# Performance work log

Hardware: AMD Instinct MI355X
Metric: run time of the kernel (lower is better)

## Reference

```python
import jax, jax.numpy as jnp
import numpy as np

N = 16384          # number of units
K = 655
BOOST_STRENGTH = 1.0


def setup_inputs() -> dict:
    key = jax.random.key(0)
    k1, k2 = jax.random.split(key)
    x = jax.random.normal(k1, (4096, N), dtype=jnp.float32)
    dutyCycle = jax.random.uniform(k2, (N,), dtype=jnp.float32)
    return {"x": x, "dutyCycle": dutyCycle}


def reference(x, dutyCycle):
    # boost factor per unit: encourages under-used units
    targetDensity = K / x.shape[1]
    boostFactors = jnp.exp((targetDensity - dutyCycle) * BOOST_STRENGTH)  # (N,)
    boosted = x * boostFactors  # (B, N)
    # top-k per row, then scatter a binary mask of winners
    _, idx = jax.lax.top_k(boosted, K)  # (B, K)
    b = jnp.arange(x.shape[0])[:, None]  # (B, 1)
    res = jnp.zeros_like(x).at[b, idx].set(1.0)
    return res
```

## Files before the change

kernel.cpp:

```cpp
#include <hip/hip_runtime.h>
#include <math.h>
#include <stdint.h>


#define N_UNITS 16384
#define K_WIN 655
#define NT 512
#define NPROBE 11
#define CAP 2048
#define ITERS (N_UNITS / (NT * 4))

__device__ __forceinline__ uint32_t fkey(float f) {
    uint32_t b = __float_as_uint(f);
    uint32_t m = (uint32_t)((int32_t)b >> 31) | 0x80000000u;
    return b ^ m;
}

__global__ void boost_kernel(const float* __restrict__ duty,
                             float* __restrict__ bf, int n) {
    int i = blockIdx.x * blockDim.x + threadIdx.x;
    if (i < n) {
        const float td = 0.03997802734375f;
        float s = td - duty[i];
        bf[i] = (float)exp((double)s);
    }
}

__global__ __launch_bounds__(NT, 6) void kwinners_kernel(
    const float* __restrict__ x, const float* __restrict__ bf,
    float* __restrict__ out) {
    __shared__ uint32_t red[(NT / 64) * NPROBE];
    __shared__ int cglob[NPROBE];
    __shared__ int prb[NPROBE];
    __shared__ uint32_t cand_idx[CAP];
    __shared__ uint32_t cand_key[CAP];
    __shared__ int sc[1];

    const int tid = threadIdx.x;
    const int lane = tid & 63;
    const int w = tid >> 6;
    const int row = blockIdx.x;
    const float4* xrow = (const float4*)(x + (size_t)row * N_UNITS);
    const float4* bfv = (const float4*)bf;
    float* orow = out + (size_t)row * N_UNITS;

    if (tid == 0) sc[0] = 0;

    int P[NPROBE];
    {
        const float pv[NPROBE] = {1.90f, 1.70f, 1.55f, 1.43f, 1.33f, 1.25f,
                                  1.18f, 1.12f, 1.06f, 0.99f, 0.90f};
#pragma unroll
        for (int p = 0; p < NPROBE; ++p) P[p] = (int)(fkey(pv[p]) >> 16);
    }

    int cnt[NPROBE];
#pragma unroll
    for (int p = 0; p < NPROBE; ++p) cnt[p] = 0;

    uint2 kh[ITERS];

#pragma unroll
    for (int j = 0; j < ITERS; ++j) {
        int i4 = tid + j * NT;
        float4 xv = xrow[i4];
        float4 bv = bfv[i4];
        int h0 = (int)(fkey(xv.x * bv.x) >> 16);
        int h1 = (int)(fkey(xv.y * bv.y) >> 16);
        int h2 = (int)(fkey(xv.z * bv.z) >> 16);
        int h3 = (int)(fkey(xv.w * bv.w) >> 16);
        kh[j].x = (uint32_t)h0 | ((uint32_t)h1 << 16);
        kh[j].y = (uint32_t)h2 | ((uint32_t)h3 << 16);
#pragma unroll
        for (int p = 0; p < NPROBE; ++p)
            cnt[p] += __popcll(__ballot(h0 > P[p])) +
                      __popcll(__ballot(h1 > P[p])) +
                      __popcll(__ballot(h2 > P[p])) +
                      __popcll(__ballot(h3 > P[p]));
    }

    auto reduce_counts = [&]() {
        if (lane == 0) {
#pragma unroll
            for (int p = 0; p < NPROBE; ++p)
                red[w * NPROBE + p] = (uint32_t)cnt[p];
        }
        __syncthreads();
        if (tid < NPROBE) {
            int s = 0;
#pragma unroll
            for (int ww = 0; ww < NT / 64; ++ww) s += (int)red[ww * NPROBE + tid];
            cglob[tid] = s;
        }
        __syncthreads();
    };
    reduce_counts();

    int lo, hi, cab, cgl;
    {
        int j = 0;
        while (j < NPROBE && cglob[j] < K_WIN) ++j;
        if (j == 0) {
            lo = P[0]; cgl = cglob[0]; hi = 65535; cab = 0;
        } else if (j == NPROBE) {
            lo = -1; cgl = N_UNITS; hi = P[NPROBE - 1]; cab = cglob[NPROBE - 1];
        } else {
            lo = P[j]; cgl = cglob[j]; hi = P[j - 1]; cab = cglob[j - 1];
        }
    }
    int m = cgl - cab;

    while (m > CAP && (hi - lo) > 1) {
        __syncthreads();
        if (tid < NPROBE)
            prb[tid] = lo + (int)(((long)(hi - lo) * (NPROBE - tid)) / (NPROBE + 1));
        __syncthreads();
#pragma unroll
        for (int p = 0; p < NPROBE; ++p) P[p] = prb[p];
#pragma unroll
        for (int p = 0; p < NPROBE; ++p) cnt[p] = 0;
#pragma unroll
        for (int j = 0; j < ITERS; ++j) {
            int h0 = (int)(kh[j].x & 0xFFFFu), h1 = (int)(kh[j].x >> 16);
            int h2 = (int)(kh[j].y & 0xFFFFu), h3 = (int)(kh[j].y >> 16);
#pragma unroll
            for (int p = 0; p < NPROBE; ++p)
                cnt[p] += __popcll(__ballot(h0 > P[p])) +
                          __popcll(__ballot(h1 > P[p])) +
                          __popcll(__ballot(h2 > P[p])) +
                          __popcll(__ballot(h3 > P[p]));
        }
        reduce_counts();
        int j = 0;
        while (j < NPROBE && cglob[j] < K_WIN) ++j;
        if (j == 0) {
            lo = P[0]; cgl = cglob[0];
        } else if (j == NPROBE) {
            hi = P[NPROBE - 1]; cab = cglob[NPROBE - 1];
        } else {
            lo = P[j]; cgl = cglob[j]; hi = P[j - 1]; cab = cglob[j - 1];
        }
        m = cgl - cab;
    }

#pragma unroll
    for (int j = 0; j < ITERS; ++j) {
        int f = tid + j * NT;
        int h0 = (int)(kh[j].x & 0xFFFFu), h1 = (int)(kh[j].x >> 16);
        int h2 = (int)(kh[j].y & 0xFFFFu), h3 = (int)(kh[j].y >> 16);
        float4 o;
        o.x = (h0 > hi) ? 1.0f : 0.0f;
        o.y = (h1 > hi) ? 1.0f : 0.0f;
        o.z = (h2 > hi) ? 1.0f : 0.0f;
        o.w = (h3 > hi) ? 1.0f : 0.0f;
        ((float4*)orow)[f] = o;
        int base = f * 4;
        int h[4] = {h0, h1, h2, h3};
#pragma unroll
        for (int e = 0; e < 4; ++e) {
            if (h[e] > lo && h[e] <= hi) {
                int p = atomicAdd(&sc[0], 1);
                if (p < CAP) cand_idx[p] = (uint32_t)(base + e);
            }
        }
    }
    __syncthreads();
    const int mm = sc[0];
    const int need = K_WIN - cab;

    const float* xr = x + (size_t)row * N_UNITS;
    const int mc = (mm <= CAP) ? mm : 0;
    for (int j = tid; j < mc; j += NT) {
        int i = (int)cand_idx[j];
        cand_key[j] = fkey(xr[i] * bf[i]);
    }
    __syncthreads();

    if (mm <= CAP) {
        for (int j = tid; j < mm; j += NT) {
            uint32_t myk = cand_key[j];
            uint32_t myi = cand_idx[j];
            int r = 0;
            for (int l = 0; l < mm; ++l) {
                uint32_t lk = cand_key[l];
                r += (lk > myk) || (lk == myk && cand_idx[l] < myi);
            }
            if (r < need) orow[myi] = 1.0f;
        }
    } else if (tid == 0) {
        uint32_t* h8 = cand_idx;
        for (int b = 0; b < 256; ++b) h8[b] = 0;
        for (int i = 0; i < N_UNITS; ++i) {
            uint32_t kf = fkey(xr[i] * bf[i]);
            if ((int)(kf >> 16) == hi) h8[(kf & 0xFFFFu) >> 8]++;
        }
        int acc = 0, d1 = 0, need2 = 0;
        for (int b = 255; b >= 0; --b) {
            int c = (int)h8[b];
            if (acc + c >= need) { d1 = b; need2 = need - acc; break; }
            acc += c;
        }
        for (int b = 0; b < 256; ++b) h8[b] = 0;
        for (int i = 0; i < N_UNITS; ++i) {
            uint32_t kf = fkey(xr[i] * bf[i]);
            if ((int)(kf >> 16) == hi && (int)((kf & 0xFFFFu) >> 8) == d1)
                h8[kf & 0xFFu]++;
        }
        int acc2 = 0, d2 = 0, need3 = 0;
        for (int b = 255; b >= 0; --b) {
            int c = (int)h8[b];
            if (acc2 + c >= need2) { d2 = b; need3 = need2 - acc2; break; }
            acc2 += c;
        }
        uint32_t Tlo = ((uint32_t)d1 << 8) | (uint32_t)d2;
        int r = 0;
        for (int i = 0; i < N_UNITS; ++i) {
            uint32_t kf = fkey(xr[i] * bf[i]);
            if ((int)(kf >> 16) == hi) {
                uint32_t kl = kf & 0xFFFFu;
                if (kl > Tlo) orow[i] = 1.0f;
                else if (kl == Tlo && r < need3) { orow[i] = 1.0f; ++r; }
            }
        }
    }
}

extern "C" void kernel_launch(void* const* d_in, const int* in_sizes, int n_in,
                              void* d_out, int out_size, void* d_ws,
                              size_t ws_size, hipStream_t stream) {
    const float* x = (const float*)d_in[0];
    const float* duty = (const float*)d_in[1];
    float* out = (float*)d_out;
    float* bf = (float*)d_ws;

    hipLaunchKernelGGL(boost_kernel, dim3(N_UNITS / 256), dim3(256), 0, stream,
                       duty, bf, N_UNITS);
    int rows = out_size / N_UNITS;
    hipLaunchKernelGGL(kwinners_kernel, dim3(rows), dim3(NT), 0, stream, x, bf,
                       out);
}
```

Before: 503.2 us.

## Refine candidate threshold with multi-probe counting before small rank sort

Replaces the O(m^2) rank computation over up to 2048 candidates with repeated 11-way threshold probing on the full 32-bit keys. This narrows the boundary bucket to at most about 64 elements, which are then ranked pairwise in a small shared buffer. Per-thread scalar counts reduced by wave shuffles replace the ballot/popcount counting. Probe thresholds are now computed in registers instead of passing through shared memory with extra barriers. Launch bounds rise to 8 waves per SIMD, which adds register pressure and the risk of spills.

Result: slower. 857.7 us (+70.4%).

```diff
diff --git a/kernel.cpp b/kernel.cpp
--- a/kernel.cpp
+++ b/kernel.cpp
@@ -8,6 +8,7 @@
 #define NT 512
 #define NPROBE 11
 #define CAP 2048
+#define SCAP 128
 #define ITERS (N_UNITS / (NT * 4))
 
 __device__ __forceinline__ uint32_t fkey(float f) {
@@ -26,15 +27,16 @@
     }
 }
 
-__global__ __launch_bounds__(NT, 6) void kwinners_kernel(
+__global__ __launch_bounds__(NT, 8) void kwinners_kernel(
     const float* __restrict__ x, const float* __restrict__ bf,
     float* __restrict__ out) {
     __shared__ uint32_t red[(NT / 64) * NPROBE];
     __shared__ int cglob[NPROBE];
-    __shared__ int prb[NPROBE];
     __shared__ uint32_t cand_idx[CAP];
     __shared__ uint32_t cand_key[CAP];
-    __shared__ int sc[1];
+    __shared__ uint32_t s_idx[SCAP];
+    __shared__ uint32_t s_key[SCAP];
+    __shared__ int sc[2];
 
     const int tid = threadIdx.x;
     const int lane = tid & 63;
@@ -44,7 +46,7 @@
     const float4* bfv = (const float4*)bf;
     float* orow = out + (size_t)row * N_UNITS;
 
-    if (tid == 0) sc[0] = 0;
+    if (tid == 0) { sc[0] = 0; sc[1] = 0; }
 
     int P[NPROBE];
     {
@@ -73,17 +75,16 @@
         kh[j].y = (uint32_t)h2 | ((uint32_t)h3 << 16);
 #pragma unroll
         for (int p = 0; p < NPROBE; ++p)
-            cnt[p] += __popcll(__ballot(h0 > P[p])) +
-                      __popcll(__ballot(h1 > P[p])) +
-                      __popcll(__ballot(h2 > P[p])) +
-                      __popcll(__ballot(h3 > P[p]));
+            cnt[p] += (h0 > P[p]) + (h1 > P[p]) + (h2 > P[p]) + (h3 > P[p]);
     }
 
     auto reduce_counts = [&]() {
-        if (lane == 0) {
-#pragma unroll
-            for (int p = 0; p < NPROBE; ++p)
-                red[w * NPROBE + p] = (uint32_t)cnt[p];
+#pragma unroll
+        for (int p = 0; p < NPROBE; ++p) {
+            int v = cnt[p];
+#pragma unroll
+            for (int m2 = 32; m2 >= 1; m2 >>= 1) v += __shfl_xor(v, m2, 64);
+            if (lane == 0) red[w * NPROBE + p] = (uint32_t)v;
         }
         __syncthreads();
         if (tid < NPROBE) {
@@ -111,12 +112,9 @@
     int m = cgl - cab;
 
     while (m > CAP && (hi - lo) > 1) {
-        __syncthreads();
-        if (tid < NPROBE)
-            prb[tid] = lo + (int)(((long)(hi - lo) * (NPROBE - tid)) / (NPROBE + 1));
-        __syncthreads();
-#pragma unroll
-        for (int p = 0; p < NPROBE; ++p) P[p] = prb[p];
+#pragma unroll
+        for (int p = 0; p < NPROBE; ++p)
+            P[p] = lo + (int)(((long)(hi - lo) * (NPROBE - p)) / (NPROBE + 1));
 #pragma unroll
         for (int p = 0; p < NPROBE; ++p) cnt[p] = 0;
 #pragma unroll
@@ -125,10 +123,7 @@
             int h2 = (int)(kh[j].y & 0xFFFFu), h3 = (int)(kh[j].y >> 16);
 #pragma unroll
             for (int p = 0; p < NPROBE; ++p)
-                cnt[p] += __popcll(__ballot(h0 > P[p])) +
-                          __popcll(__ballot(h1 > P[p])) +
-                          __popcll(__ballot(h2 > P[p])) +
-                          __popcll(__ballot(h3 > P[p]));
+                cnt[p] += (h0 > P[p]) + (h1 > P[p]) + (h2 > P[p]) + (h3 > P[p]);
         }
         reduce_counts();
         int j = 0;
@@ -177,15 +172,77 @@
     __syncthreads();
 
     if (mm <= CAP) {
+        long gLo = -1, gHi = 0xFFFFFFFFL;
+        int cHi = 0, cGL = mm;
+        int inB = mm, guard = 0;
+        while (inB > 64 && (gHi - gLo) > 1 && ++guard <= 40) {
+            long T[NPROBE];
+            unsigned long range = (unsigned long)(gHi - gLo);
+#pragma unroll
+            for (int p = 0; p < NPROBE; ++p)
+                T[p] = gLo + (long)(range * (unsigned long)(NPROBE - p) /
+                                    (NPROBE + 1));
+#pragma unroll
+            for (int p = 0; p < NPROBE; ++p) cnt[p] = 0;
+            for (int j = tid; j < mm; j += NT) {
+                long k = (long)cand_key[j];
+#pragma unroll
+                for (int p = 0; p < NPROBE; ++p) cnt[p] += (k > T[p]);
+            }
+            reduce_counts();
+            int j = 0;
+            while (j < NPROBE && cglob[j] < need) ++j;
+            if (j == 0) {
+                gLo = T[0]; cGL = cglob[0];
+            } else if (j == NPROBE) {
+                gHi = T[NPROBE - 1]; cHi = cglob[NPROBE - 1];
+            } else {
+                gLo = T[j]; cGL = cglob[j]; gHi = T[j - 1]; cHi = cglob[j - 1];
+            }
+            inB = cGL - cHi;
+        }
+        const int need2 = need - cHi;
+
         for (int j = tid; j < mm; j += NT) {
-            uint32_t myk = cand_key[j];
-            uint32_t myi = cand_idx[j];
-            int r = 0;
-            for (int l = 0; l < mm; ++l) {
-                uint32_t lk = cand_key[l];
-                r += (lk > myk) || (lk == myk && cand_idx[l] < myi);
-            }
-            if (r < need) orow[myi] = 1.0f;
+            long k = (long)cand_key[j];
+            if (k > gHi) {
+                orow[cand_idx[j]] = 1.0f;
+            } else if (k > gLo) {
+                int p = atomicAdd(&sc[1], 1);
+                if (p < SCAP) { s_key[p] = cand_key[j]; s_idx[p] = cand_idx[j]; }
+            }
+        }
+        __syncthreads();
+        const int sS = sc[1];
+
+        if (sS <= SCAP) {
+            for (int j = tid; j < sS; j += NT) {
+                uint32_t myk = s_key[j];
+                uint32_t myi = s_idx[j];
+                int r = 0;
+                for (int l = 0; l < sS; ++l) {
+                    uint32_t lk = s_key[l];
+                    r += (lk > myk) || (lk == myk && s_idx[l] < myi);
+                }
+                if (r < need2) orow[myi] = 1.0f;
+            }
+        } else {
+            for (int j = tid; j < mm; j += NT) {
+                long k = (long)cand_key[j];
+                if (k > gLo && k <= gHi) {
+                    uint32_t myk = cand_key[j];
+                    uint32_t myi = cand_idx[j];
+                    int r = 0;
+                    for (int l = 0; l < mm; ++l) {
+                        long lk2 = (long)cand_key[l];
+                        if (lk2 > gLo && lk2 <= gHi) {
+                            uint32_t lk = cand_key[l];
+                            r += (lk > myk) || (lk == myk && cand_idx[l] < myi);
+                        }
+                    }
+                    if (r < need2) orow[myi] = 1.0f;
+                }
+            }
         }
     } else if (tid == 0) {
         uint32_t* h8 = cand_idx;
```

## Refine full 32-bit threshold in registers and write mask once via shared bitmap

Applied to the files above, without the earlier changes.

Keeps full 32-bit sort keys in registers instead of 16-bit halves. The multi-probe threshold search now runs down to a bucket of at most 128 candidates, counting per thread and reducing with shuffles instead of ballot/popcount. Boundary winners are recorded in a shared bitmap so the output row is written once, with no global re-read or scattered overwrites. The cost is twice the key registers per thread (possible occupancy loss) and possibly more refinement passes over register data.

Result: slower. 650.3 us (+29.2%).

```diff
diff --git a/kernel.cpp b/kernel.cpp
--- a/kernel.cpp
+++ b/kernel.cpp
@@ -7,7 +7,7 @@
 #define K_WIN 655
 #define NT 512
 #define NPROBE 11
-#define CAP 2048
+#define SCAP 128
 #define ITERS (N_UNITS / (NT * 4))
 
 __device__ __forceinline__ uint32_t fkey(float f) {
@@ -31,9 +31,9 @@
     float* __restrict__ out) {
     __shared__ uint32_t red[(NT / 64) * NPROBE];
     __shared__ int cglob[NPROBE];
-    __shared__ int prb[NPROBE];
-    __shared__ uint32_t cand_idx[CAP];
-    __shared__ uint32_t cand_key[CAP];
+    __shared__ uint32_t s_key[SCAP];
+    __shared__ uint32_t s_idx[SCAP];
+    __shared__ uint32_t bmap[N_UNITS / 32];
     __shared__ int sc[1];
 
     const int tid = threadIdx.x;
@@ -44,46 +44,45 @@
     const float4* bfv = (const float4*)bf;
     float* orow = out + (size_t)row * N_UNITS;
 
+    bmap[tid] = 0u;
     if (tid == 0) sc[0] = 0;
 
-    int P[NPROBE];
+    uint32_t PF[NPROBE];
     {
         const float pv[NPROBE] = {1.90f, 1.70f, 1.55f, 1.43f, 1.33f, 1.25f,
                                   1.18f, 1.12f, 1.06f, 0.99f, 0.90f};
 #pragma unroll
-        for (int p = 0; p < NPROBE; ++p) P[p] = (int)(fkey(pv[p]) >> 16);
+        for (int p = 0; p < NPROBE; ++p) PF[p] = fkey(pv[p]) | 0xFFFFu;
     }
 
     int cnt[NPROBE];
 #pragma unroll
     for (int p = 0; p < NPROBE; ++p) cnt[p] = 0;
 
-    uint2 kh[ITERS];
+    uint4 kk[ITERS];
 
 #pragma unroll
     for (int j = 0; j < ITERS; ++j) {
         int i4 = tid + j * NT;
         float4 xv = xrow[i4];
         float4 bv = bfv[i4];
-        int h0 = (int)(fkey(xv.x * bv.x) >> 16);
-        int h1 = (int)(fkey(xv.y * bv.y) >> 16);
-        int h2 = (int)(fkey(xv.z * bv.z) >> 16);
-        int h3 = (int)(fkey(xv.w * bv.w) >> 16);
-        kh[j].x = (uint32_t)h0 | ((uint32_t)h1 << 16);
-        kh[j].y = (uint32_t)h2 | ((uint32_t)h3 << 16);
+        kk[j].x = fkey(xv.x * bv.x);
+        kk[j].y = fkey(xv.y * bv.y);
+        kk[j].z = fkey(xv.z * bv.z);
+        kk[j].w = fkey(xv.w * bv.w);
 #pragma unroll
         for (int p = 0; p < NPROBE; ++p)
-            cnt[p] += __popcll(__ballot(h0 > P[p])) +
-                      __popcll(__ballot(h1 > P[p])) +
-                      __popcll(__ballot(h2 > P[p])) +
-                      __popcll(__ballot(h3 > P[p]));
+            cnt[p] += (kk[j].x > PF[p]) + (kk[j].y > PF[p]) +
+                      (kk[j].z > PF[p]) + (kk[j].w > PF[p]);
     }
 
     auto reduce_counts = [&]() {
-        if (lane == 0) {
-#pragma unroll
-            for (int p = 0; p < NPROBE; ++p)
-                red[w * NPROBE + p] = (uint32_t)cnt[p];
+#pragma unroll
+        for (int p = 0; p < NPROBE; ++p) {
+            int v = cnt[p];
+#pragma unroll
+            for (int m2 = 32; m2 >= 1; m2 >>= 1) v += __shfl_xor(v, m2, 64);
+            if (lane == 0) red[w * NPROBE + p] = (uint32_t)v;
         }
         __syncthreads();
         if (tid < NPROBE) {
@@ -96,132 +95,111 @@
     };
     reduce_counts();
 
-    int lo, hi, cab, cgl;
+    long lo, hi;
+    int cab, cgl;
     {
         int j = 0;
         while (j < NPROBE && cglob[j] < K_WIN) ++j;
         if (j == 0) {
-            lo = P[0]; cgl = cglob[0]; hi = 65535; cab = 0;
+            lo = (long)PF[0]; cgl = cglob[0]; hi = 0xFFFFFFFFL; cab = 0;
         } else if (j == NPROBE) {
-            lo = -1; cgl = N_UNITS; hi = P[NPROBE - 1]; cab = cglob[NPROBE - 1];
+            lo = -1; cgl = N_UNITS; hi = (long)PF[NPROBE - 1];
+            cab = cglob[NPROBE - 1];
         } else {
-            lo = P[j]; cgl = cglob[j]; hi = P[j - 1]; cab = cglob[j - 1];
-        }
-    }
-    int m = cgl - cab;
-
-    while (m > CAP && (hi - lo) > 1) {
-        __syncthreads();
-        if (tid < NPROBE)
-            prb[tid] = lo + (int)(((long)(hi - lo) * (NPROBE - tid)) / (NPROBE + 1));
-        __syncthreads();
-#pragma unroll
-        for (int p = 0; p < NPROBE; ++p) P[p] = prb[p];
-#pragma unroll
-        for (int p = 0; p < NPROBE; ++p) cnt[p] = 0;
-#pragma unroll
-        for (int j = 0; j < ITERS; ++j) {
-            int h0 = (int)(kh[j].x & 0xFFFFu), h1 = (int)(kh[j].x >> 16);
-            int h2 = (int)(kh[j].y & 0xFFFFu), h3 = (int)(kh[j].y >> 16);
-#pragma unroll
-            for (int p = 0; p < NPROBE; ++p)
-                cnt[p] += __popcll(__ballot(h0 > P[p])) +
-                          __popcll(__ballot(h1 > P[p])) +
-                          __popcll(__ballot(h2 > P[p])) +
-                          __popcll(__ballot(h3 > P[p]));
+            lo = (long)PF[j]; cgl = cglob[j]; hi = (long)PF[j - 1];
+            cab = cglob[j - 1];
+        }
+    }
+    int inB = cgl - cab;
+
+    while (inB > SCAP && (hi - lo) > 1) {
+        unsigned long range = (unsigned long)(hi - lo);
+#pragma unroll
+        for (int p = 0; p < NPROBE; ++p) {
+            long Tp = lo + (long)(range * (unsigned long)(NPROBE - p) /
+                                  (NPROBE + 1));
+            int c = 0;
+#pragma unroll
+            for (int j = 0; j < ITERS; ++j)
+                c += ((long)kk[j].x > Tp) + ((long)kk[j].y > Tp) +
+                     ((long)kk[j].z > Tp) + ((long)kk[j].w > Tp);
+            cnt[p] = c;
         }
         reduce_counts();
         int j = 0;
         while (j < NPROBE && cglob[j] < K_WIN) ++j;
+        const long llo = lo;
+        auto Tof = [&](int p) {
+            return llo + (long)(range * (unsigned long)(NPROBE - p) /
+                                (NPROBE + 1));
+        };
         if (j == 0) {
-            lo = P[0]; cgl = cglob[0];
+            lo = Tof(0); cgl = cglob[0];
         } else if (j == NPROBE) {
-            hi = P[NPROBE - 1]; cab = cglob[NPROBE - 1];
+            hi = Tof(NPROBE - 1); cab = cglob[NPROBE - 1];
         } else {
-            lo = P[j]; cgl = cglob[j]; hi = P[j - 1]; cab = cglob[j - 1];
-        }
-        m = cgl - cab;
-    }
+            lo = Tof(j); cgl = cglob[j]; hi = Tof(j - 1); cab = cglob[j - 1];
+        }
+        inB = cgl - cab;
+    }
+    const int need = K_WIN - cab;
+
+    if (inB <= SCAP) {
+#pragma unroll
+        for (int j = 0; j < ITERS; ++j) {
+            int base = (tid + j * NT) * 4;
+            uint32_t kv[4] = {kk[j].x, kk[j].y, kk[j].z, kk[j].w};
+#pragma unroll
+            for (int e = 0; e < 4; ++e) {
+                long k = (long)kv[e];
+                if (k > lo && k <= hi) {
+                    int p = atomicAdd(&sc[0], 1);
+                    if (p < SCAP) {
+                        s_key[p] = kv[e];
+                        s_idx[p] = (uint32_t)(base + e);
+                    }
+                }
+            }
+        }
+        __syncthreads();
+        const int sS = sc[0];
+
+        for (int jj = tid; jj < sS; jj += NT) {
+            uint32_t myk = s_key[jj];
+            uint32_t myi = s_idx[jj];
+            int r = 0;
+            for (int l = 0; l < sS; ++l) {
+                uint32_t lk = s_key[l];
+                r += (lk > myk) || (lk == myk && s_idx[l] < myi);
+            }
+            if (r < need) atomicOr(&bmap[myi >> 5], 1u << (myi & 31));
+        }
+    } else {
+        if (tid == 0) {
+            const float* xr = x + (size_t)row * N_UNITS;
+            int r = 0;
+            for (int i = 0; i < N_UNITS && r < need; ++i) {
+                uint32_t kf = fkey(xr[i] * bf[i]);
+                if ((long)kf == hi) {
+                    bmap[i >> 5] |= (1u << (i & 31));
+                    ++r;
+                }
+            }
+        }
+    }
+    __syncthreads();
 
 #pragma unroll
     for (int j = 0; j < ITERS; ++j) {
         int f = tid + j * NT;
-        int h0 = (int)(kh[j].x & 0xFFFFu), h1 = (int)(kh[j].x >> 16);
-        int h2 = (int)(kh[j].y & 0xFFFFu), h3 = (int)(kh[j].y >> 16);
+        uint32_t bm = bmap[f >> 3];
+        int sh = (f & 7) * 4;
         float4 o;
-        o.x = (h0 > hi) ? 1.0f : 0.0f;
-        o.y = (h1 > hi) ? 1.0f : 0.0f;
-        o.z = (h2 > hi) ? 1.0f : 0.0f;
-        o.w = (h3 > hi) ? 1.0f : 0.0f;
+        o.x = (((long)kk[j].x > hi) || ((bm >> (sh + 0)) & 1u)) ? 1.0f : 0.0f;
+        o.y = (((long)kk[j].y > hi) || ((bm >> (sh + 1)) & 1u)) ? 1.0f : 0.0f;
+        o.z = (((long)kk[j].z > hi) || ((bm >> (sh + 2)) & 1u)) ? 1.0f : 0.0f;
+        o.w = (((long)kk[j].w > hi) || ((bm >> (sh + 3)) & 1u)) ? 1.0f : 0.0f;
         ((float4*)orow)[f] = o;
-        int base = f * 4;
-        int h[4] = {h0, h1, h2, h3};
-#pragma unroll
-        for (int e = 0; e < 4; ++e) {
-            if (h[e] > lo && h[e] <= hi) {
-                int p = atomicAdd(&sc[0], 1);
-                if (p < CAP) cand_idx[p] = (uint32_t)(base + e);
-            }
-        }
-    }
-    __syncthreads();
-    const int mm = sc[0];
-    const int need = K_WIN - cab;
-
-    const float* xr = x + (size_t)row * N_UNITS;
-    const int mc = (mm <= CAP) ? mm : 0;
-    for (int j = tid; j < mc; j += NT) {
-        int i = (int)cand_idx[j];
-        cand_key[j] = fkey(xr[i] * bf[i]);
-    }
-    __syncthreads();
-
-    if (mm <= CAP) {
-        for (int j = tid; j < mm; j += NT) {
-            uint32_t myk = cand_key[j];
-            uint32_t myi = cand_idx[j];
-            int r = 0;
-            for (int l = 0; l < mm; ++l) {
-                uint32_t lk = cand_key[l];
-                r += (lk > myk) || (lk == myk && cand_idx[l] < myi);
-            }
-            if (r < need) orow[myi] = 1.0f;
-        }
-    } else if (tid == 0) {
-        uint32_t* h8 = cand_idx;
-        for (int b = 0; b < 256; ++b) h8[b] = 0;
-        for (int i = 0; i < N_UNITS; ++i) {
-            uint32_t kf = fkey(xr[i] * bf[i]);
-            if ((int)(kf >> 16) == hi) h8[(kf & 0xFFFFu) >> 8]++;
-        }
-        int acc = 0, d1 = 0, need2 = 0;
-        for (int b = 255; b >= 0; --b) {
-            int c = (int)h8[b];
-            if (acc + c >= need) { d1 = b; need2 = need - acc; break; }
-            acc += c;
-        }
-        for (int b = 0; b < 256; ++b) h8[b] = 0;
-        for (int i = 0; i < N_UNITS; ++i) {
-            uint32_t kf = fkey(xr[i] * bf[i]);
-            if ((int)(kf >> 16) == hi && (int)((kf & 0xFFFFu) >> 8) == d1)
-                h8[kf & 0xFFu]++;
-        }
-        int acc2 = 0, d2 = 0, need3 = 0;
-        for (int b = 255; b >= 0; --b) {
-            int c = (int)h8[b];
-            if (acc2 + c >= need2) { d2 = b; need3 = need2 - acc2; break; }
-            acc2 += c;
-        }
-        uint32_t Tlo = ((uint32_t)d1 << 8) | (uint32_t)d2;
-        int r = 0;
-        for (int i = 0; i < N_UNITS; ++i) {
-            uint32_t kf = fkey(xr[i] * bf[i]);
-            if ((int)(kf >> 16) == hi) {
-                uint32_t kl = kf & 0xFFFFu;
-                if (kl > Tlo) orow[i] = 1.0f;
-                else if (kl == Tlo && r < need3) { orow[i] = 1.0f; ++r; }
-            }
-        }
     }
 }
 
```
